# Kernel tuning notes

Measured on AMD Instinct MI355X. Metric: run time of the kernel, lower is better.

## Reference

```python
import jax, jax.numpy as jnp
import numpy as np

DIM = 128
H = 8
HD = DIM // H
NL = 6
DFF = 2048
EPS = 1e-5
S2S_STEPS = 6


def _ln(x, g, b):
    m = jnp.mean(x, -1, keepdims=True)
    v = jnp.mean(jnp.square(x - m), -1, keepdims=True)
    return (x - m) / jnp.sqrt(v + EPS) * g + b


def _lstm_step(x, h, c, wih, whh, bih, bhh):
    # torch LSTM gate order: i, f, g, o
    gates = x @ wih.T + bih + h @ whh.T + bhh
    i, f, g, o = jnp.split(gates, 4, axis=-1)
    c = jax.nn.sigmoid(f) * c + jax.nn.sigmoid(i) * jnp.tanh(g)
    h = jax.nn.sigmoid(o) * jnp.tanh(c)
    return h, c


def setup_inputs() -> dict:
    key = jax.random.key(0)
    ks = iter(jax.random.split(key, 16))
    n = lambda shape: jax.random.normal(next(ks), shape, jnp.float32) * 0.02
    inp = {
        "data": jax.random.normal(next(ks), (64, 256, 3), jnp.float32),
        "lin0_w": n((DIM, 3)), "lin0_b": jnp.zeros((DIM,), jnp.float32),
        "attn_in_w": n((NL, 3 * DIM, DIM)), "attn_in_b": jnp.zeros((NL, 3 * DIM), jnp.float32),
        "attn_out_w": n((NL, DIM, DIM)), "attn_out_b": jnp.zeros((NL, DIM), jnp.float32),
        "ln1_g": jnp.ones((NL, DIM), jnp.float32), "ln1_b": jnp.zeros((NL, DIM), jnp.float32),
        "ff_w1": n((NL, DFF, DIM)), "ff_b1": jnp.zeros((NL, DFF), jnp.float32),
        "ff_w2": n((NL, DIM, DFF)), "ff_b2": jnp.zeros((NL, DIM), jnp.float32),
        "ln2_g": jnp.ones((NL, DIM), jnp.float32), "ln2_b": jnp.zeros((NL, DIM), jnp.float32),
        "s2s_wih": n((4 * DIM, 2 * DIM)), "s2s_whh": n((4 * DIM, DIM)),
        "s2s_bih": jnp.zeros((4 * DIM,), jnp.float32), "s2s_bhh": jnp.zeros((4 * DIM,), jnp.float32),
        "mem_wih": n((4 * DIM, 2 * DIM)), "mem_whh": n((4 * DIM, DIM)),
        "mem_bih": jnp.zeros((4 * DIM,), jnp.float32), "mem_bhh": jnp.zeros((4 * DIM,), jnp.float32),
        "lin1_w": n((DIM, DIM)), "lin1_b": jnp.zeros((DIM,), jnp.float32),
        "lin3_w": n((1, DIM)), "lin3_b": jnp.zeros((1,), jnp.float32),
    }
    return inp


def reference(data, lin0_w, lin0_b, attn_in_w, attn_in_b, attn_out_w, attn_out_b,
              ln1_g, ln1_b, ff_w1, ff_b1, ff_w2, ff_b2, ln2_g, ln2_b,
              s2s_wih, s2s_whh, s2s_bih, s2s_bhh,
              mem_wih, mem_whh, mem_bih, mem_bhh,
              lin1_w, lin1_b, lin3_w, lin3_b):
    x = jax.nn.relu(data @ lin0_w.T + lin0_b)  # [S=64, B=256, D]
    S, B, _ = x.shape
    # torch TransformerEncoder with batch_first=False: attention over axis 0,
    # axis 1 is the transformer batch. Post-norm layers (norm_first=False), relu FFN.
    for l in range(NL):
        qkv = x @ attn_in_w[l].T + attn_in_b[l]
        q, k, v = jnp.split(qkv, 3, axis=-1)
        q = q.reshape(S, B, H, HD)
        k = k.reshape(S, B, H, HD)
        v = v.reshape(S, B, H, HD)
        scores = jnp.einsum('sbhd,tbhd->bhst', q, k) / np.float32(np.sqrt(HD))
        attn = jax.nn.softmax(scores, axis=-1)
        ao = jnp.einsum('bhst,tbhd->sbhd', attn, v).reshape(S, B, DIM)
        x = _ln(x + ao @ attn_out_w[l].T + attn_out_b[l], ln1_g[l], ln1_b[l])
        ff = jax.nn.relu(x @ ff_w1[l].T + ff_b1[l]) @ ff_w2[l].T + ff_b2[l]
        x = _ln(x + ff, ln2_g[l], ln2_b[l])
    # Set2Set pooling: bidxs assign segment = axis-0 index for each block of
    # num_atoms consecutive rows of flatten(out,0,1), i.e. pool over axis 1.
    q_star = jnp.zeros((S, 2 * DIM), x.dtype)
    h = jnp.zeros((S, DIM), x.dtype)
    c = jnp.zeros((S, DIM), x.dtype)
    for _ in range(S2S_STEPS):
        h, c = _lstm_step(q_star, h, c, s2s_wih, s2s_whh, s2s_bih, s2s_bhh)
        e = jnp.einsum('bnd,bd->bn', x, h)          # [S, num_atoms]
        a = jax.nn.softmax(e, axis=-1)              # segment softmax (uniform segs)
        r = jnp.einsum('bn,bnd->bd', a, x)          # segment weighted sum
        q_star = jnp.concatenate([h, r], axis=-1)   # [S, 2D]
    # memory LSTM: seq_len 1, zero initial state (states=None branch)
    hx = jnp.zeros((S, DIM), x.dtype)
    cx = jnp.zeros((S, DIM), x.dtype)
    hx, cx = _lstm_step(q_star, hx, cx, mem_wih, mem_whh, mem_bih, mem_bhh)
    o = jax.nn.relu(hx @ lin1_w.T + lin1_b)
    v_out = (o @ lin3_w.T + lin3_b)[None]  # [1, S, 1]
    return v_out, hx[None], cx[None]
```

## Files before the change

kernel.cpp:

```cpp
#include <hip/hip_runtime.h>
#include <math.h>


typedef __attribute__((ext_vector_type(8))) short bf16x8;
typedef __attribute__((ext_vector_type(4))) float f32x4;
typedef _Float16 __attribute__((ext_vector_type(2))) h16x2;

__device__ __forceinline__ unsigned short f2bf(float f) {
  union { float f; unsigned u; } x; x.f = f;
  unsigned r = x.u + 0x7fff + ((x.u >> 16) & 1);
  return (unsigned short)(r >> 16);
}
__device__ __forceinline__ float uplo(unsigned u) {
  union { unsigned u; float f; } x; x.u = u << 16; return x.f;
}
__device__ __forceinline__ float uphi(unsigned u) {
  union { unsigned u; float f; } x; x.u = u & 0xffff0000u; return x.f;
}
__device__ __forceinline__ unsigned short f2h(float f) {
  union { _Float16 h; unsigned short s; } x; x.h = (_Float16)f; return x.s;
}
__device__ __forceinline__ unsigned packh(float a, float b) {
  return (unsigned)f2h(a) | ((unsigned)f2h(b) << 16);
}
__device__ __forceinline__ float hlo(unsigned u) {
  union { unsigned short s; _Float16 h; } x; x.s = (unsigned short)(u & 0xffff);
  return (float)x.h;
}
__device__ __forceinline__ float hhi(unsigned u) {
  union { unsigned short s; _Float16 h; } x; x.s = (unsigned short)(u >> 16);
  return (float)x.h;
}
__device__ __forceinline__ float fdot2u(unsigned a, unsigned b, float c) {
#if __has_builtin(__builtin_amdgcn_fdot2)
  union U { unsigned u; h16x2 h; };
  U x, y; x.u = a; y.u = b;
  return __builtin_amdgcn_fdot2(x.h, y.h, c, false);
#else
  return c + hlo(a) * hlo(b) + hhi(a) * hhi(b);
#endif
}
__device__ __forceinline__ float sigf(float x) { return 1.f / (1.f + expf(-x)); }

__device__ __forceinline__ void gl2lds16(const void* g, void* l) {
  __builtin_amdgcn_global_load_lds(
      (const __attribute__((address_space(1))) unsigned int*)g,
      (__attribute__((address_space(3))) unsigned int*)l, 16, 0, 0);
}

__global__ __launch_bounds__(256) void convw_kernel(
    const float* __restrict__ aiw, const float* __restrict__ aow,
    const float* __restrict__ w1, const float* __restrict__ w2,
    const float* __restrict__ wih, const float* __restrict__ whh,
    const float* __restrict__ mwih,
    unsigned short* __restrict__ o0, unsigned short* __restrict__ o1,
    unsigned short* __restrict__ o2, unsigned short* __restrict__ o3,
    unsigned short* __restrict__ o4, unsigned short* __restrict__ o5,
    unsigned short* __restrict__ o6) {
  int i = blockIdx.x * 256 + threadIdx.x;
  if (i < 294912) {
    o0[i] = f2bf(aiw[i]);
  } else if (i < 393216) {
    int j = i - 294912; o1[j] = f2bf(aow[j]);
  } else if (i < 1966080) {
    int j = i - 393216; o2[j] = f2bf(w1[j]);
  } else if (i < 3538944) {
    int j = i - 1966080; o3[j] = f2bf(w2[j]);
  } else if (i < 3670016) {
    int j = i - 3538944; o4[j] = f2h(wih[j]);
  } else if (i < 3735552) {
    int j = i - 3670016; o5[j] = f2h(whh[j]);
  } else {
    int j = i - 3735552; o6[j] = f2h(mwih[j]);
  }
}

__global__ __launch_bounds__(256) void lin0_kernel(
    const float* __restrict__ data, const float* __restrict__ w,
    const float* __restrict__ b, float* __restrict__ x,
    unsigned short* __restrict__ xb) {
  int i = blockIdx.x * 256 + threadIdx.x;
  int n = i >> 7, d = i & 127;
  float v = b[d] + data[n * 3 + 0] * w[d * 3 + 0]
                 + data[n * 3 + 1] * w[d * 3 + 1]
                 + data[n * 3 + 2] * w[d * 3 + 2];
  v = fmaxf(v, 0.0f);
  x[i] = v;
  xb[i] = f2bf(v);
}

__global__ __launch_bounds__(512) void layer_kernel(
    const unsigned short* __restrict__ xbg,
    const unsigned short* __restrict__ wqkv, const float* __restrict__ bqkv,
    const unsigned short* __restrict__ wout, const float* __restrict__ bout,
    const float* __restrict__ ln1g, const float* __restrict__ ln1b,
    const unsigned short* __restrict__ w1, const float* __restrict__ b1,
    const unsigned short* __restrict__ w2, const float* __restrict__ b2,
    const float* __restrict__ ln2g, const float* __restrict__ ln2b,
    float* __restrict__ xio, unsigned short* __restrict__ xbo) {
  __shared__ __align__(16) unsigned short Xs[64 * 128];
  __shared__ __align__(16) unsigned short Ws[256 * 128];
  __shared__ __align__(16) unsigned short U1[128 * 128];
  __shared__ __align__(16) unsigned short U2[128 * 128];
  __shared__ __align__(16) uint4 zchunk;
  __shared__ float psum[8][64], psq[8][64];
  __shared__ float2 stats[64];

  unsigned short* Qs = U1;
  unsigned short* Ks2 = U1 + 8192;
  unsigned short* VT = U2;
  unsigned short* AOs = U2 + 8192;
  unsigned short* Hs = U2;

  int tid = threadIdx.x, w = tid >> 6, lane = tid & 63;
  int b = blockIdx.x;
  int r4 = lane >> 4, cs = lane & 15;
  int fr = lane & 15, fq = lane >> 4;

  if (tid == 0) zchunk = make_uint4(0u, 0u, 0u, 0u);

#pragma unroll
  for (int i = 0; i < 2; i++) {
    int issue = w * 2 + i;
    int row = issue * 4 + r4;
    int g = cs ^ (row & 7);
    gl2lds16(xbg + (size_t)(row * 256 + b) * 128 + g * 8,
             (char*)Xs + issue * 1024);
  }
#pragma unroll
  for (int i = 0; i < 8; i++) {
    int issue = w * 8 + i;
    int row = issue * 4 + r4;
    int g = cs ^ (row & 7);
    gl2lds16(wqkv + (size_t)row * 128 + g * 8, (char*)Ws + issue * 1024);
  }
  __syncthreads();

  {
    f32x4 acc[4][2];
#pragma unroll
    for (int i = 0; i < 4; i++)
#pragma unroll
      for (int j = 0; j < 2; j++) acc[i][j] = (f32x4){0.f, 0.f, 0.f, 0.f};
#pragma unroll
    for (int ks = 0; ks < 4; ks++) {
      bf16x8 af[4], bf[2];
#pragma unroll
      for (int mi = 0; mi < 4; mi++) {
        int row = mi * 16 + fr;
        int kq = (ks * 4 + fq) ^ (row & 7);
        af[mi] = *(const bf16x8*)(Xs + row * 128 + kq * 8);
      }
#pragma unroll
      for (int ni = 0; ni < 2; ni++) {
        int wr = (w * 2 + ni) * 16 + fr;
        int kq = (ks * 4 + fq) ^ (wr & 7);
        bf[ni] = *(const bf16x8*)(Ws + wr * 128 + kq * 8);
      }
#pragma unroll
      for (int mi = 0; mi < 4; mi++)
#pragma unroll
        for (int ni = 0; ni < 2; ni++)
          acc[mi][ni] = __builtin_amdgcn_mfma_f32_16x16x32_bf16(
              af[mi], bf[ni], acc[mi][ni], 0, 0, 0);
    }
#pragma unroll
    for (int ni = 0; ni < 2; ni++) {
      int c = (w * 2 + ni) * 16 + fr;
      float bv = bqkv[c];
      unsigned short* dst = (c < 128) ? Qs : Ks2;
      int cc = c & 127;
#pragma unroll
      for (int mi = 0; mi < 4; mi++)
#pragma unroll
        for (int r = 0; r < 4; r++) {
          int row = mi * 16 + fq * 4 + r;
          dst[row * 128 + (((cc >> 3) ^ (row & 7)) << 3) + (cc & 7)] =
              f2bf(acc[mi][ni][r] + bv);
        }
    }
  }
  __syncthreads();

#pragma unroll
  for (int i = 0; i < 4; i++) {
    int issue = w * 4 + i;
    int row = issue * 4 + r4;
    int g = cs ^ (row & 7);
    gl2lds16(wqkv + (size_t)(256 + row) * 128 + g * 8, (char*)Ws + issue * 1024);
  }
  __syncthreads();

  {
    f32x4 acc[4];
#pragma unroll
    for (int i = 0; i < 4; i++) acc[i] = (f32x4){0.f, 0.f, 0.f, 0.f};
#pragma unroll
    for (int ks = 0; ks < 4; ks++) {
      bf16x8 af[4], bf;
#pragma unroll
      for (int mi = 0; mi < 4; mi++) {
        int row = mi * 16 + fr;
        int kq = (ks * 4 + fq) ^ (row & 7);
        af[mi] = *(const bf16x8*)(Xs + row * 128 + kq * 8);
      }
      {
        int wr = w * 16 + fr;
        int kq = (ks * 4 + fq) ^ (wr & 7);
        bf = *(const bf16x8*)(Ws + wr * 128 + kq * 8);
      }
#pragma unroll
      for (int mi = 0; mi < 4; mi++)
        acc[mi] = __builtin_amdgcn_mfma_f32_16x16x32_bf16(af[mi], bf, acc[mi],
                                                          0, 0, 0);
    }
    int f = w * 16 + fr;
    float bv = bqkv[256 + f];
#pragma unroll
    for (int mi = 0; mi < 4; mi++)
#pragma unroll
      for (int r = 0; r < 4; r++) {
        int srow = mi * 16 + fq * 4 + r;
        VT[f * 64 + (((srow >> 3) ^ (f & 7)) << 3) + (srow & 7)] =
            f2bf(acc[mi][r] + bv);
      }
  }
  __syncthreads();

  {
    int h = w;
    unsigned short* Pb = Ws + w * 4096;
    f32x4 sc[4][4];
#pragma unroll
    for (int i = 0; i < 4; i++)
#pragma unroll
      for (int j = 0; j < 4; j++) sc[i][j] = (f32x4){0.f, 0.f, 0.f, 0.f};
    {
      bf16x8 af[4], bf[4];
#pragma unroll
      for (int mi = 0; mi < 4; mi++) {
        int row = mi * 16 + fr;
        const unsigned short* pa =
            (fq < 2) ? (Qs + row * 128 + (((h * 2 + fq) ^ (row & 7)) << 3))
                     : (const unsigned short*)&zchunk;
        af[mi] = *(const bf16x8*)pa;
      }
#pragma unroll
      for (int ti = 0; ti < 4; ti++) {
        int trow = ti * 16 + fr;
        const unsigned short* pb =
            (fq < 2) ? (Ks2 + trow * 128 + (((h * 2 + fq) ^ (trow & 7)) << 3))
                     : (const unsigned short*)&zchunk;
        bf[ti] = *(const bf16x8*)pb;
      }
#pragma unroll
      for (int mi = 0; mi < 4; mi++)
#pragma unroll
        for (int ti = 0; ti < 4; ti++)
          sc[mi][ti] = __builtin_amdgcn_mfma_f32_16x16x32_bf16(
              af[mi], bf[ti], sc[mi][ti], 0, 0, 0);
    }
#pragma unroll
    for (int mi = 0; mi < 4; mi++) {
#pragma unroll
      for (int r = 0; r < 4; r++) {
        float m = -1e30f;
#pragma unroll
        for (int ti = 0; ti < 4; ti++) m = fmaxf(m, sc[mi][ti][r]);
        m = fmaxf(m, __shfl_xor(m, 1, 64));
        m = fmaxf(m, __shfl_xor(m, 2, 64));
        m = fmaxf(m, __shfl_xor(m, 4, 64));
        m = fmaxf(m, __shfl_xor(m, 8, 64));
        m *= 0.25f;
        float ss = 0.f;
#pragma unroll
        for (int ti = 0; ti < 4; ti++) {
          float p = expf(sc[mi][ti][r] * 0.25f - m);
          sc[mi][ti][r] = p;
          ss += p;
        }
        ss += __shfl_xor(ss, 1, 64);
        ss += __shfl_xor(ss, 2, 64);
        ss += __shfl_xor(ss, 4, 64);
        ss += __shfl_xor(ss, 8, 64);
        float inv = 1.f / ss;
        int prow = mi * 16 + fq * 4 + r;
#pragma unroll
        for (int ti = 0; ti < 4; ti++) {
          int t = ti * 16 + fr;
          Pb[prow * 64 + (((t >> 3) ^ (prow & 7)) << 3) + (t & 7)] =
              f2bf(sc[mi][ti][r] * inv);
        }
      }
    }
    f32x4 po[4];
#pragma unroll
    for (int i = 0; i < 4; i++) po[i] = (f32x4){0.f, 0.f, 0.f, 0.f};
#pragma unroll
    for (int ks2 = 0; ks2 < 2; ks2++) {
      bf16x8 af[4], bf;
#pragma unroll
      for (int si = 0; si < 4; si++) {
        int prow = si * 16 + fr;
        int kq = (ks2 * 4 + fq) ^ (prow & 7);
        af[si] = *(const bf16x8*)(Pb + prow * 64 + kq * 8);
      }
      {
        int vrow = h * 16 + fr;
        int kq = (ks2 * 4 + fq) ^ (vrow & 7);
        bf = *(const bf16x8*)(VT + vrow * 64 + kq * 8);
      }
#pragma unroll
      for (int si = 0; si < 4; si++)
        po[si] = __builtin_amdgcn_mfma_f32_16x16x32_bf16(af[si], bf, po[si],
                                                         0, 0, 0);
    }
#pragma unroll
    for (int si = 0; si < 4; si++)
#pragma unroll
      for (int r = 0; r < 4; r++) {
        int arow = si * 16 + fq * 4 + r;
        int c = h * 16 + fr;
        AOs[arow * 128 + (((c >> 3) ^ (arow & 7)) << 3) + (c & 7)] =
            f2bf(po[si][r]);
      }
  }
  __syncthreads();

#pragma unroll
  for (int i = 0; i < 4; i++) {
    int issue = w * 4 + i;
    int row = issue * 4 + r4;
    int g = cs ^ (row & 7);
    gl2lds16(wout + (size_t)row * 128 + g * 8, (char*)Ws + issue * 1024);
  }
  __syncthreads();

  float vvl[4][4];
  {
    f32x4 acc[4];
#pragma unroll
    for (int i = 0; i < 4; i++) acc[i] = (f32x4){0.f, 0.f, 0.f, 0.f};
#pragma unroll
    for (int ks = 0; ks < 4; ks++) {
      bf16x8 af[4], bf;
#pragma unroll
      for (int si = 0; si < 4; si++) {
        int row = si * 16 + fr;
        int kq = (ks * 4 + fq) ^ (row & 7);
        af[si] = *(const bf16x8*)(AOs + row * 128 + kq * 8);
      }
      {
        int wr = w * 16 + fr;
        int kq = (ks * 4 + fq) ^ (wr & 7);
        bf = *(const bf16x8*)(Ws + wr * 128 + kq * 8);
      }
#pragma unroll
      for (int si = 0; si < 4; si++)
        acc[si] = __builtin_amdgcn_mfma_f32_16x16x32_bf16(af[si], bf, acc[si],
                                                          0, 0, 0);
    }
    int c = w * 16 + fr;
    float bv = bout[c];
    float sums[4][4], sqs[4][4];
#pragma unroll
    for (int si = 0; si < 4; si++)
#pragma unroll
      for (int r = 0; r < 4; r++) {
        int row = si * 16 + fq * 4 + r;
        float v = acc[si][r] + bv + xio[(size_t)(row * 256 + b) * 128 + c];
        vvl[si][r] = v;
        sums[si][r] = v;
        sqs[si][r] = v * v;
      }
#pragma unroll
    for (int d = 1; d < 16; d <<= 1) {
#pragma unroll
      for (int si = 0; si < 4; si++)
#pragma unroll
        for (int r = 0; r < 4; r++) {
          sums[si][r] += __shfl_xor(sums[si][r], d, 64);
          sqs[si][r] += __shfl_xor(sqs[si][r], d, 64);
        }
    }
    if (fr == 0) {
#pragma unroll
      for (int si = 0; si < 4; si++)
#pragma unroll
        for (int r = 0; r < 4; r++) {
          int row = si * 16 + fq * 4 + r;
          psum[w][row] = sums[si][r];
          psq[w][row] = sqs[si][r];
        }
    }
    __syncthreads();
    if (tid < 64) {
      float S = 0.f, Q = 0.f;
#pragma unroll
      for (int ww = 0; ww < 8; ww++) { S += psum[ww][tid]; Q += psq[ww][tid]; }
      float m = S * (1.f / 128.f);
      float var = Q * (1.f / 128.f) - m * m;
      stats[tid] = make_float2(m, rsqrtf(var + 1e-5f));
    }
    __syncthreads();
    float gl = ln1g[c], bl = ln1b[c];
#pragma unroll
    for (int si = 0; si < 4; si++)
#pragma unroll
      for (int r = 0; r < 4; r++) {
        int row = si * 16 + fq * 4 + r;
        float2 st = stats[row];
        float y = (vvl[si][r] - st.x) * st.y * gl + bl;
        vvl[si][r] = y;
        Xs[row * 128 + (((c >> 3) ^ (row & 7)) << 3) + (c & 7)] = f2bf(y);
      }
  }

#pragma unroll
  for (int i = 0; i < 4; i++) {
    int issue = w * 4 + i;
    int row = issue * 4 + r4;
    int g = cs ^ (row & 7);
    gl2lds16(w1 + (size_t)row * 128 + g * 8, (char*)Ws + issue * 1024);
    gl2lds16(w2 + (size_t)row * 2048 + g * 8, (char*)U1 + issue * 1024);
  }
  __syncthreads();

  f32x4 acc2[4];
#pragma unroll
  for (int i = 0; i < 4; i++) acc2[i] = (f32x4){0.f, 0.f, 0.f, 0.f};

  for (int c = 0; c < 16; c++) {
    const unsigned short* W1cur = Ws + (c & 1) * 16384;
    f32x4 acc1[4];
#pragma unroll
    for (int i = 0; i < 4; i++) acc1[i] = (f32x4){0.f, 0.f, 0.f, 0.f};
#pragma unroll
    for (int ks = 0; ks < 4; ks++) {
      bf16x8 af[4], bf;
#pragma unroll
      for (int mi = 0; mi < 4; mi++) {
        int row = mi * 16 + fr;
        int kq = (ks * 4 + fq) ^ (row & 7);
        af[mi] = *(const bf16x8*)(Xs + row * 128 + kq * 8);
      }
      {
        int row = w * 16 + fr;
        int kq = (ks * 4 + fq) ^ (row & 7);
        bf = *(const bf16x8*)(W1cur + row * 128 + kq * 8);
      }
#pragma unroll
      for (int mi = 0; mi < 4; mi++)
        acc1[mi] = __builtin_amdgcn_mfma_f32_16x16x32_bf16(af[mi], bf, acc1[mi],
                                                           0, 0, 0);
    }
    if (c < 15) {
#pragma unroll
      for (int i = 0; i < 4; i++) {
        int issue = w * 4 + i;
        int row = issue * 4 + r4;
        int g = cs ^ (row & 7);
        gl2lds16(w1 + (size_t)((c + 1) * 128 + row) * 128 + g * 8,
                 (char*)Ws + ((c + 1) & 1) * 32768 + issue * 1024);
      }
    }
    {
      int col = w * 16 + fr;
      float bv = b1[c * 128 + col];
#pragma unroll
      for (int mi = 0; mi < 4; mi++)
#pragma unroll
        for (int r = 0; r < 4; r++) {
          int row = mi * 16 + fq * 4 + r;
          Hs[row * 136 + col] = f2bf(fmaxf(acc1[mi][r] + bv, 0.f));
        }
    }
    __syncthreads();

#pragma unroll
    for (int ks = 0; ks < 4; ks++) {
      bf16x8 af[4], bf;
#pragma unroll
      for (int si = 0; si < 4; si++) {
        int row = si * 16 + fr;
        af[si] = *(const bf16x8*)(Hs + row * 136 + ks * 32 + fq * 8);
      }
      {
        int row = w * 16 + fr;
        int kq = (ks * 4 + fq) ^ (row & 7);
        bf = *(const bf16x8*)(U1 + row * 128 + kq * 8);
      }
#pragma unroll
      for (int si = 0; si < 4; si++)
        acc2[si] = __builtin_amdgcn_mfma_f32_16x16x32_bf16(af[si], bf, acc2[si],
                                                           0, 0, 0);
    }
    __syncthreads();
    if (c < 15) {
#pragma unroll
      for (int i = 0; i < 4; i++) {
        int issue = w * 4 + i;
        int row = issue * 4 + r4;
        int g = cs ^ (row & 7);
        gl2lds16(w2 + (size_t)row * 2048 + (c + 1) * 128 + g * 8,
                 (char*)U1 + issue * 1024);
      }
    }
  }

  {
    int c = w * 16 + fr;
    float bv = b2[c];
    float sums[4][4], sqs[4][4];
#pragma unroll
    for (int si = 0; si < 4; si++)
#pragma unroll
      for (int r = 0; r < 4; r++) {
        float v = acc2[si][r] + bv + vvl[si][r];
        vvl[si][r] = v;
        sums[si][r] = v;
        sqs[si][r] = v * v;
      }
#pragma unroll
    for (int d = 1; d < 16; d <<= 1) {
#pragma unroll
      for (int si = 0; si < 4; si++)
#pragma unroll
        for (int r = 0; r < 4; r++) {
          sums[si][r] += __shfl_xor(sums[si][r], d, 64);
          sqs[si][r] += __shfl_xor(sqs[si][r], d, 64);
        }
    }
    if (fr == 0) {
#pragma unroll
      for (int si = 0; si < 4; si++)
#pragma unroll
        for (int r = 0; r < 4; r++) {
          int row = si * 16 + fq * 4 + r;
          psum[w][row] = sums[si][r];
          psq[w][row] = sqs[si][r];
        }
    }
    __syncthreads();
    if (tid < 64) {
      float S = 0.f, Q = 0.f;
#pragma unroll
      for (int ww = 0; ww < 8; ww++) { S += psum[ww][tid]; Q += psq[ww][tid]; }
      float m = S * (1.f / 128.f);
      float var = Q * (1.f / 128.f) - m * m;
      stats[tid] = make_float2(m, rsqrtf(var + 1e-5f));
    }
    __syncthreads();
    float gl = ln2g[c], bl = ln2b[c];
#pragma unroll
    for (int si = 0; si < 4; si++)
#pragma unroll
      for (int r = 0; r < 4; r++) {
        int row = si * 16 + fq * 4 + r;
        float2 st = stats[row];
        float y = (vvl[si][r] - st.x) * st.y * gl + bl;
        size_t o = (size_t)(row * 256 + b) * 128 + c;
        xio[o] = y;
        xbo[o] = f2bf(y);
      }
  }
}

__global__ __launch_bounds__(512, 1) void s2s_kernel(
    const unsigned short* __restrict__ xb,
    const unsigned short* __restrict__ wihh,
    const unsigned short* __restrict__ whhh,
    const float* __restrict__ bih, const float* __restrict__ bhh,
    const unsigned short* __restrict__ mwihh,
    const float* __restrict__ mbih, const float* __restrict__ mbhh,
    const float* __restrict__ l1w, const float* __restrict__ l1b,
    const float* __restrict__ l3w, const float* __restrict__ l3b,
    float* __restrict__ out) {
  __shared__ __align__(16) unsigned xl[256 * 65];
  __shared__ __align__(16) unsigned qu[128];
  __shared__ __align__(16) float cst[128];
  __shared__ __align__(16) float gates[512];
  __shared__ __align__(16) float red[256];
  __shared__ __align__(16) float aw[256];
  int s = blockIdx.x, t = threadIdx.x, lane = t & 63, w = t >> 6;

  uint4 wreg[32], ureg[16];
  {
    const uint4* wp = (const uint4*)(wihh + (size_t)t * 256);
#pragma unroll
    for (int i = 0; i < 32; i++) wreg[i] = wp[i];
    const uint4* up = (const uint4*)(whhh + (size_t)t * 128);
#pragma unroll
    for (int i = 0; i < 16; i++) ureg[i] = up[i];
  }

  const uint4* xs4 = (const uint4*)(xb + (size_t)s * 32768);
#pragma unroll
  for (int it = 0; it < 8; it++) {
    int f = it * 512 + t;
    uint4 v = xs4[f];
    int n = f >> 4, jc = (f & 15) * 4;
    unsigned* dst = xl + n * 65 + jc;
    dst[0] = packh(uplo(v.x), uphi(v.x));
    dst[1] = packh(uplo(v.y), uphi(v.y));
    dst[2] = packh(uplo(v.z), uphi(v.z));
    dst[3] = packh(uplo(v.w), uphi(v.w));
  }
  if (t < 128) cst[t] = 0.f;
  __syncthreads();

  const uint4* q4 = (const uint4*)qu;
  float bsum = bih[t] + bhh[t];

  for (int step = 0; step < 6; step++) {
    if (step > 0) {
      float a0 = 0.f, a1 = 0.f, a2 = 0.f, a3 = 0.f;
#pragma unroll
      for (int i = 0; i < 16; i++) {
        uint4 qv = q4[i];
        a0 = fdot2u(wreg[i].x, qv.x, a0);
        a1 = fdot2u(wreg[i].y, qv.y, a1);
        a2 = fdot2u(wreg[i].z, qv.z, a2);
        a3 = fdot2u(wreg[i].w, qv.w, a3);
        a0 = fdot2u(ureg[i].x, qv.x, a0);
        a1 = fdot2u(ureg[i].y, qv.y, a1);
        a2 = fdot2u(ureg[i].z, qv.z, a2);
        a3 = fdot2u(ureg[i].w, qv.w, a3);
      }
#pragma unroll
      for (int i = 16; i < 32; i++) {
        uint4 qv = q4[i];
        a0 = fdot2u(wreg[i].x, qv.x, a0);
        a1 = fdot2u(wreg[i].y, qv.y, a1);
        a2 = fdot2u(wreg[i].z, qv.z, a2);
        a3 = fdot2u(wreg[i].w, qv.w, a3);
      }
      gates[t] = bsum + ((a0 + a1) + (a2 + a3));
    } else {
      gates[t] = bsum;
    }
    __syncthreads();
    if (t < 128) {
      float ig = sigf(gates[t]), fg = sigf(gates[128 + t]);
      float gg = tanhf(gates[256 + t]), og = sigf(gates[384 + t]);
      float cn = fg * cst[t] + ig * gg;
      cst[t] = cn;
      float hn = og * tanhf(cn);
      float hp = __shfl_xor(hn, 1, 64);
      if ((t & 1) == 0) qu[t >> 1] = packh(hn, hp);
    }
    __syncthreads();
    if (step > 0) {
      int n = t >> 1, p = t & 1;
      const unsigned* xr = xl + n * 65 + p * 32;
      float e0 = 0.f, e1 = 0.f;
#pragma unroll 8
      for (int i = 0; i < 32; i += 2) {
        e0 = fdot2u(xr[i], qu[p * 32 + i], e0);
        e1 = fdot2u(xr[i + 1], qu[p * 32 + i + 1], e1);
      }
      float e = e0 + e1;
      e += __shfl_xor(e, 1, 64);
      if (p == 0) red[n] = e;
      __syncthreads();
      float v0 = red[lane], v1 = red[64 + lane];
      float v2 = red[128 + lane], v3 = red[192 + lane];
      float m = fmaxf(fmaxf(v0, v1), fmaxf(v2, v3));
#pragma unroll
      for (int d = 1; d < 64; d <<= 1) m = fmaxf(m, __shfl_xor(m, d, 64));
      float p0 = expf(v0 - m), p1 = expf(v1 - m);
      float p2 = expf(v2 - m), p3 = expf(v3 - m);
      float ss = p0 + p1 + p2 + p3;
#pragma unroll
      for (int d = 1; d < 64; d <<= 1) ss += __shfl_xor(ss, d, 64);
      float Sinv = 1.f / ss;
      if (w == 0) {
        aw[lane] = p0 * Sinv; aw[64 + lane] = p1 * Sinv;
        aw[128 + lane] = p2 * Sinv; aw[192 + lane] = p3 * Sinv;
      }
    } else {
      if (t < 256) aw[t] = 1.f / 256.f;
    }
    __syncthreads();
    {
      int d = t & 127, grp = t >> 7;
      const unsigned* xc = xl + grp * 64 * 65 + (d >> 1);
      int hi = d & 1;
      const float* ap = aw + grp * 64;
      float r = 0.f;
#pragma unroll 8
      for (int n2 = 0; n2 < 64; n2++) {
        unsigned u = xc[n2 * 65];
        r += ap[n2] * (hi ? hhi(u) : hlo(u));
      }
      gates[t] = r;
    }
    __syncthreads();
    if (t < 128) {
      float rd = gates[t] + gates[128 + t] + gates[256 + t] + gates[384 + t];
      float rp = __shfl_xor(rd, 1, 64);
      if ((t & 1) == 0) qu[64 + (t >> 1)] = packh(rd, rp);
    }
    __syncthreads();
  }
  {
    float a0 = 0.f, a1 = 0.f, a2 = 0.f, a3 = 0.f;
    const uint4* mp = (const uint4*)(mwihh + (size_t)t * 256);
#pragma unroll 8
    for (int i = 0; i < 32; i++) {
      uint4 wv = mp[i], qv = q4[i];
      a0 = fdot2u(wv.x, qv.x, a0);
      a1 = fdot2u(wv.y, qv.y, a1);
      a2 = fdot2u(wv.z, qv.z, a2);
      a3 = fdot2u(wv.w, qv.w, a3);
    }
    gates[t] = mbih[t] + mbhh[t] + ((a0 + a1) + (a2 + a3));
  }
  __syncthreads();
  if (t < 128) {
    float ig = sigf(gates[t]);
    float gg = tanhf(gates[256 + t]);
    float og = sigf(gates[384 + t]);
    float cx = ig * gg;
    float hx = og * tanhf(cx);
    cst[t] = hx;
    out[64 + s * 128 + t] = hx;
    out[64 + 8192 + s * 128 + t] = cx;
  }
  __syncthreads();
  if (t < 128) {
    float acc = l1b[t];
    const float4* w4 = (const float4*)(l1w + (size_t)t * 128);
    const float4* h4 = (const float4*)cst;
#pragma unroll 8
    for (int k = 0; k < 32; k++) {
      float4 a = w4[k], b = h4[k];
      acc += a.x * b.x + a.y * b.y + a.z * b.z + a.w * b.w;
    }
    red[t] = fmaxf(acc, 0.f) * l3w[t];
  } else if (t < 256) {
    red[t] = 0.f;
  }
  __syncthreads();
  for (int off = 128; off; off >>= 1) {
    if (t < off) red[t] += red[t + off];
    __syncthreads();
  }
  if (t == 0) out[s] = red[0] + l3b[0];
}

extern "C" void kernel_launch(void* const* d_in, const int* in_sizes, int n_in,
                              void* d_out, int out_size, void* d_ws,
                              size_t ws_size, hipStream_t stream) {
  const float* data       = (const float*)d_in[0];
  const float* lin0_w     = (const float*)d_in[1];
  const float* lin0_b     = (const float*)d_in[2];
  const float* attn_in_w  = (const float*)d_in[3];
  const float* attn_in_b  = (const float*)d_in[4];
  const float* attn_out_w = (const float*)d_in[5];
  const float* attn_out_b = (const float*)d_in[6];
  const float* ln1_g      = (const float*)d_in[7];
  const float* ln1_b      = (const float*)d_in[8];
  const float* ff_w1      = (const float*)d_in[9];
  const float* ff_b1      = (const float*)d_in[10];
  const float* ff_w2      = (const float*)d_in[11];
  const float* ff_b2      = (const float*)d_in[12];
  const float* ln2_g      = (const float*)d_in[13];
  const float* ln2_b      = (const float*)d_in[14];
  const float* s2s_wih    = (const float*)d_in[15];
  const float* s2s_whh    = (const float*)d_in[16];
  const float* s2s_bih    = (const float*)d_in[17];
  const float* s2s_bhh    = (const float*)d_in[18];
  const float* mem_wih    = (const float*)d_in[19];
  const float* mem_bih    = (const float*)d_in[21];
  const float* mem_bhh    = (const float*)d_in[22];
  const float* lin1_w     = (const float*)d_in[23];
  const float* lin1_b     = (const float*)d_in[24];
  const float* lin3_w     = (const float*)d_in[25];
  const float* lin3_b     = (const float*)d_in[26];
  float* out = (float*)d_out;

  char* p = (char*)d_ws;
  float* x = (float*)p;                      p += (size_t)16384 * 128 * 4;
  unsigned short* xb = (unsigned short*)p;   p += (size_t)16384 * 128 * 2;
  unsigned short* wqkv = (unsigned short*)p; p += (size_t)294912 * 2;
  unsigned short* wout = (unsigned short*)p; p += (size_t)98304 * 2;
  unsigned short* w1b = (unsigned short*)p;  p += (size_t)1572864 * 2;
  unsigned short* w2b = (unsigned short*)p;  p += (size_t)1572864 * 2;
  unsigned short* wihh = (unsigned short*)p; p += (size_t)131072 * 2;
  unsigned short* whhh = (unsigned short*)p; p += (size_t)65536 * 2;
  unsigned short* mwihh = (unsigned short*)p; p += (size_t)131072 * 2;

  convw_kernel<<<15104, 256, 0, stream>>>(
      attn_in_w, attn_out_w, ff_w1, ff_w2, s2s_wih, s2s_whh, mem_wih,
      wqkv, wout, w1b, w2b, wihh, whhh, mwihh);
  lin0_kernel<<<8192, 256, 0, stream>>>(data, lin0_w, lin0_b, x, xb);

  for (int l = 0; l < 6; l++) {
    layer_kernel<<<256, 512, 0, stream>>>(
        xb, wqkv + (size_t)l * 49152, attn_in_b + l * 384,
        wout + (size_t)l * 16384, attn_out_b + l * 128,
        ln1_g + l * 128, ln1_b + l * 128,
        w1b + (size_t)l * 262144, ff_b1 + l * 2048,
        w2b + (size_t)l * 262144, ff_b2 + l * 128,
        ln2_g + l * 128, ln2_b + l * 128, x, xb);
  }

  s2s_kernel<<<64, 512, 0, stream>>>(
      xb, wihh, whhh, s2s_bih, s2s_bhh,
      mwihh, mem_bih, mem_bhh, lin1_w, lin1_b, lin3_w, lin3_b, out);
}
```

Measured before the change: 504.0 us.

## Keep FFN hidden activations in registers via transposed fp16 MFMA chaining

Result: slower. 530.2 us (+5.2%).

```diff
diff --git a/kernel.cpp b/kernel.cpp
--- a/kernel.cpp
+++ b/kernel.cpp
@@ -5,11 +5,16 @@
 typedef __attribute__((ext_vector_type(8))) short bf16x8;
 typedef __attribute__((ext_vector_type(4))) float f32x4;
 typedef _Float16 __attribute__((ext_vector_type(2))) h16x2;
+typedef _Float16 __attribute__((ext_vector_type(4))) f16x4;
 
 __device__ __forceinline__ unsigned short f2bf(float f) {
   union { float f; unsigned u; } x; x.f = f;
   unsigned r = x.u + 0x7fff + ((x.u >> 16) & 1);
   return (unsigned short)(r >> 16);
+}
+__device__ __forceinline__ float bf2f(unsigned short u) {
+  union { unsigned u; float f; } x; x.u = ((unsigned)u) << 16;
+  return x.f;
 }
 __device__ __forceinline__ float uplo(unsigned u) {
   union { unsigned u; float f; } x; x.u = u << 16; return x.f;
@@ -65,7 +70,7 @@
   } else if (i < 1966080) {
     int j = i - 393216; o2[j] = f2bf(w1[j]);
   } else if (i < 3538944) {
-    int j = i - 1966080; o3[j] = f2bf(w2[j]);
+    int j = i - 1966080; o3[j] = f2h(w2[j]);
   } else if (i < 3670016) {
     int j = i - 3538944; o4[j] = f2h(wih[j]);
   } else if (i < 3735552) {
@@ -110,7 +115,6 @@
   unsigned short* Ks2 = U1 + 8192;
   unsigned short* VT = U2;
   unsigned short* AOs = U2 + 8192;
-  unsigned short* Hs = U2;
 
   int tid = threadIdx.x, w = tid >> 6, lane = tid & 63;
   int b = blockIdx.x;
@@ -336,7 +340,6 @@
   }
   __syncthreads();
 
-  float vvl[4][4];
   {
     f32x4 acc[4];
 #pragma unroll
@@ -362,6 +365,7 @@
     }
     int c = w * 16 + fr;
     float bv = bout[c];
+    float vv4[4][4];
     float sums[4][4], sqs[4][4];
 #pragma unroll
     for (int si = 0; si < 4; si++)
@@ -369,7 +373,7 @@
       for (int r = 0; r < 4; r++) {
         int row = si * 16 + fq * 4 + r;
         float v = acc[si][r] + bv + xio[(size_t)(row * 256 + b) * 128 + c];
-        vvl[si][r] = v;
+        vv4[si][r] = v;
         sums[si][r] = v;
         sqs[si][r] = v * v;
       }
@@ -394,6 +398,15 @@
         }
     }
     __syncthreads();
+
+#pragma unroll
+    for (int i = 0; i < 4; i++) {
+      int issue = w * 4 + i;
+      int row = issue * 4 + r4;
+      int g = cs ^ (row & 7);
+      gl2lds16(w1 + (size_t)row * 128 + g * 8, (char*)Ws + issue * 1024);
+      gl2lds16(w2 + (size_t)row * 2048 + g * 8, (char*)U1 + issue * 1024);
+    }
     if (tid < 64) {
       float S = 0.f, Q = 0.f;
 #pragma unroll
@@ -409,51 +422,23 @@
 #pragma unroll
       for (int r = 0; r < 4; r++) {
         int row = si * 16 + fq * 4 + r;
-        float2 st = stats[row];
-        float y = (vvl[si][r] - st.x) * st.y * gl + bl;
-        vvl[si][r] = y;
+        float2 st2 = stats[row];
+        float y = (vv4[si][r] - st2.x) * st2.y * gl + bl;
         Xs[row * 128 + (((c >> 3) ^ (row & 7)) << 3) + (c & 7)] = f2bf(y);
       }
   }
-
-#pragma unroll
-  for (int i = 0; i < 4; i++) {
-    int issue = w * 4 + i;
-    int row = issue * 4 + r4;
-    int g = cs ^ (row & 7);
-    gl2lds16(w1 + (size_t)row * 128 + g * 8, (char*)Ws + issue * 1024);
-    gl2lds16(w2 + (size_t)row * 2048 + g * 8, (char*)U1 + issue * 1024);
-  }
-  __syncthreads();
-
-  f32x4 acc2[4];
-#pragma unroll
-  for (int i = 0; i < 4; i++) acc2[i] = (f32x4){0.f, 0.f, 0.f, 0.f};
+  __syncthreads();
+
+  int st = w >> 1;
+  int hh = w & 1;
+
+  f32x4 acc2[8];
+#pragma unroll
+  for (int i = 0; i < 8; i++) acc2[i] = (f32x4){0.f, 0.f, 0.f, 0.f};
 
   for (int c = 0; c < 16; c++) {
     const unsigned short* W1cur = Ws + (c & 1) * 16384;
-    f32x4 acc1[4];
-#pragma unroll
-    for (int i = 0; i < 4; i++) acc1[i] = (f32x4){0.f, 0.f, 0.f, 0.f};
-#pragma unroll
-    for (int ks = 0; ks < 4; ks++) {
-      bf16x8 af[4], bf;
-#pragma unroll
-      for (int mi = 0; mi < 4; mi++) {
-        int row = mi * 16 + fr;
-        int kq = (ks * 4 + fq) ^ (row & 7);
-        af[mi] = *(const bf16x8*)(Xs + row * 128 + kq * 8);
-      }
-      {
-        int row = w * 16 + fr;
-        int kq = (ks * 4 + fq) ^ (row & 7);
-        bf = *(const bf16x8*)(W1cur + row * 128 + kq * 8);
-      }
-#pragma unroll
-      for (int mi = 0; mi < 4; mi++)
-        acc1[mi] = __builtin_amdgcn_mfma_f32_16x16x32_bf16(af[mi], bf, acc1[mi],
-                                                           0, 0, 0);
-    }
+    const unsigned short* W2cur = (c & 1) ? U2 : U1;
     if (c < 15) {
 #pragma unroll
       for (int i = 0; i < 4; i++) {
@@ -462,107 +447,94 @@
         int g = cs ^ (row & 7);
         gl2lds16(w1 + (size_t)((c + 1) * 128 + row) * 128 + g * 8,
                  (char*)Ws + ((c + 1) & 1) * 32768 + issue * 1024);
-      }
-    }
-    {
-      int col = w * 16 + fr;
-      float bv = b1[c * 128 + col];
-#pragma unroll
-      for (int mi = 0; mi < 4; mi++)
-#pragma unroll
-        for (int r = 0; r < 4; r++) {
-          int row = mi * 16 + fq * 4 + r;
-          Hs[row * 136 + col] = f2bf(fmaxf(acc1[mi][r] + bv, 0.f));
-        }
-    }
-    __syncthreads();
-
-#pragma unroll
-    for (int ks = 0; ks < 4; ks++) {
-      bf16x8 af[4], bf;
-#pragma unroll
-      for (int si = 0; si < 4; si++) {
-        int row = si * 16 + fr;
-        af[si] = *(const bf16x8*)(Hs + row * 136 + ks * 32 + fq * 8);
-      }
-      {
-        int row = w * 16 + fr;
-        int kq = (ks * 4 + fq) ^ (row & 7);
-        bf = *(const bf16x8*)(U1 + row * 128 + kq * 8);
-      }
-#pragma unroll
-      for (int si = 0; si < 4; si++)
-        acc2[si] = __builtin_amdgcn_mfma_f32_16x16x32_bf16(af[si], bf, acc2[si],
-                                                           0, 0, 0);
-    }
-    __syncthreads();
-    if (c < 15) {
-#pragma unroll
-      for (int i = 0; i < 4; i++) {
-        int issue = w * 4 + i;
-        int row = issue * 4 + r4;
-        int g = cs ^ (row & 7);
         gl2lds16(w2 + (size_t)row * 2048 + (c + 1) * 128 + g * 8,
-                 (char*)U1 + issue * 1024);
-      }
-    }
-  }
-
-  {
-    int c = w * 16 + fr;
-    float bv = b2[c];
-    float sums[4][4], sqs[4][4];
-#pragma unroll
-    for (int si = 0; si < 4; si++)
-#pragma unroll
-      for (int r = 0; r < 4; r++) {
-        float v = acc2[si][r] + bv + vvl[si][r];
-        vvl[si][r] = v;
-        sums[si][r] = v;
-        sqs[si][r] = v * v;
-      }
-#pragma unroll
-    for (int d = 1; d < 16; d <<= 1) {
-#pragma unroll
-      for (int si = 0; si < 4; si++)
-#pragma unroll
-        for (int r = 0; r < 4; r++) {
-          sums[si][r] += __shfl_xor(sums[si][r], d, 64);
-          sqs[si][r] += __shfl_xor(sqs[si][r], d, 64);
-        }
-    }
-    if (fr == 0) {
-#pragma unroll
-      for (int si = 0; si < 4; si++)
-#pragma unroll
-        for (int r = 0; r < 4; r++) {
-          int row = si * 16 + fq * 4 + r;
-          psum[w][row] = sums[si][r];
-          psq[w][row] = sqs[si][r];
-        }
-    }
-    __syncthreads();
-    if (tid < 64) {
-      float S = 0.f, Q = 0.f;
-#pragma unroll
-      for (int ww = 0; ww < 8; ww++) { S += psum[ww][tid]; Q += psq[ww][tid]; }
-      float m = S * (1.f / 128.f);
-      float var = Q * (1.f / 128.f) - m * m;
-      stats[tid] = make_float2(m, rsqrtf(var + 1e-5f));
-    }
-    __syncthreads();
-    float gl = ln2g[c], bl = ln2b[c];
-#pragma unroll
-    for (int si = 0; si < 4; si++)
-#pragma unroll
-      for (int r = 0; r < 4; r++) {
-        int row = si * 16 + fq * 4 + r;
-        float2 st = stats[row];
-        float y = (vvl[si][r] - st.x) * st.y * gl + bl;
-        size_t o = (size_t)(row * 256 + b) * 128 + c;
-        xio[o] = y;
-        xbo[o] = f2bf(y);
-      }
+                 (char*)((c & 1) ? U1 : U2) + issue * 1024);
+      }
+    }
+    f16x4 hf[4];
+#pragma unroll
+    for (int ht = 0; ht < 4; ht++) {
+      f32x4 a1 = (f32x4){0.f, 0.f, 0.f, 0.f};
+      int hrow = hh * 64 + ht * 16 + fr;
+      int srow = st * 16 + fr;
+#pragma unroll
+      for (int ks = 0; ks < 4; ks++) {
+        bf16x8 aw = *(const bf16x8*)(W1cur + hrow * 128 +
+                                     (((ks * 4 + fq) ^ (hrow & 7)) << 3));
+        bf16x8 bx = *(const bf16x8*)(Xs + srow * 128 +
+                                     (((ks * 4 + fq) ^ (srow & 7)) << 3));
+        a1 = __builtin_amdgcn_mfma_f32_16x16x32_bf16(aw, bx, a1, 0, 0, 0);
+      }
+      float4 b1v = *(const float4*)(b1 + c * 128 + hh * 64 + ht * 16 + fq * 4);
+      hf[ht][0] = (_Float16)fmaxf(a1[0] + b1v.x, 0.f);
+      hf[ht][1] = (_Float16)fmaxf(a1[1] + b1v.y, 0.f);
+      hf[ht][2] = (_Float16)fmaxf(a1[2] + b1v.z, 0.f);
+      hf[ht][3] = (_Float16)fmaxf(a1[3] + b1v.w, 0.f);
+    }
+#pragma unroll
+    for (int ot = 0; ot < 8; ot++) {
+#pragma unroll
+      for (int ht = 0; ht < 4; ht++) {
+        int orow = ot * 16 + fr;
+        int c16 = hh * 8 + ht * 2 + (fq >> 1);
+        f16x4 wv = *(const f16x4*)(W2cur + orow * 128 +
+                                   ((c16 ^ (orow & 7)) << 3) + (fq & 1) * 4);
+        acc2[ot] = __builtin_amdgcn_mfma_f32_16x16x16f16(wv, hf[ht], acc2[ot],
+                                                         0, 0, 0);
+      }
+    }
+    __syncthreads();
+  }
+
+  if (hh == 1) {
+    float* slot = (float*)Ws + st * 2048;
+#pragma unroll
+    for (int ot = 0; ot < 8; ot++)
+      *(f32x4*)(slot + ot * 256 + lane * 4) = acc2[ot];
+  }
+  __syncthreads();
+  if (hh == 0) {
+    const float* slot = (const float*)Ws + st * 2048;
+#pragma unroll
+    for (int ot = 0; ot < 8; ot++)
+      acc2[ot] += *(const f32x4*)(slot + ot * 256 + lane * 4);
+
+    int s = st * 16 + fr;
+    float vals[8][4];
+    float sum = 0.f, sq = 0.f;
+#pragma unroll
+    for (int ot = 0; ot < 8; ot++) {
+      int o0 = ot * 16 + fq * 4;
+      float4 b2v = *(const float4*)(b2 + o0);
+      int cx = ((o0 >> 3) ^ (s & 7));
+      ushort4 ru = *(const ushort4*)(Xs + s * 128 + (cx << 3) + (fq & 1) * 4);
+      float v0 = acc2[ot][0] + b2v.x + bf2f(ru.x);
+      float v1 = acc2[ot][1] + b2v.y + bf2f(ru.y);
+      float v2 = acc2[ot][2] + b2v.z + bf2f(ru.z);
+      float v3 = acc2[ot][3] + b2v.w + bf2f(ru.w);
+      vals[ot][0] = v0; vals[ot][1] = v1; vals[ot][2] = v2; vals[ot][3] = v3;
+      sum += (v0 + v1) + (v2 + v3);
+      sq += (v0 * v0 + v1 * v1) + (v2 * v2 + v3 * v3);
+    }
+    sum += __shfl_xor(sum, 16, 64); sum += __shfl_xor(sum, 32, 64);
+    sq += __shfl_xor(sq, 16, 64);   sq += __shfl_xor(sq, 32, 64);
+    float mean = sum * (1.f / 128.f);
+    float inv = rsqrtf(sq * (1.f / 128.f) - mean * mean + 1e-5f);
+    size_t rowbase = (size_t)(s * 256 + b) * 128;
+#pragma unroll
+    for (int ot = 0; ot < 8; ot++) {
+      int o0 = ot * 16 + fq * 4;
+      float4 g4 = *(const float4*)(ln2g + o0);
+      float4 bb4 = *(const float4*)(ln2b + o0);
+      float y0 = (vals[ot][0] - mean) * inv * g4.x + bb4.x;
+      float y1 = (vals[ot][1] - mean) * inv * g4.y + bb4.y;
+      float y2 = (vals[ot][2] - mean) * inv * g4.z + bb4.z;
+      float y3 = (vals[ot][3] - mean) * inv * g4.w + bb4.w;
+      *(float4*)(xio + rowbase + o0) = make_float4(y0, y1, y2, y3);
+      ushort4 ub;
+      ub.x = f2bf(y0); ub.y = f2bf(y1); ub.z = f2bf(y2); ub.w = f2bf(y3);
+      *(ushort4*)(xbo + rowbase + o0) = ub;
+    }
   }
 }
 
@@ -786,14 +758,14 @@
   unsigned short* wqkv = (unsigned short*)p; p += (size_t)294912 * 2;
   unsigned short* wout = (unsigned short*)p; p += (size_t)98304 * 2;
   unsigned short* w1b = (unsigned short*)p;  p += (size_t)1572864 * 2;
-  unsigned short* w2b = (unsigned short*)p;  p += (size_t)1572864 * 2;
+  unsigned short* w2h = (unsigned short*)p;  p += (size_t)1572864 * 2;
   unsigned short* wihh = (unsigned short*)p; p += (size_t)131072 * 2;
   unsigned short* whhh = (unsigned short*)p; p += (size_t)65536 * 2;
   unsigned short* mwihh = (unsigned short*)p; p += (size_t)131072 * 2;
 
   convw_kernel<<<15104, 256, 0, stream>>>(
       attn_in_w, attn_out_w, ff_w1, ff_w2, s2s_wih, s2s_whh, mem_wih,
-      wqkv, wout, w1b, w2b, wihh, whhh, mwihh);
+      wqkv, wout, w1b, w2h, wihh, whhh, mwihh);
   lin0_kernel<<<8192, 256, 0, stream>>>(data, lin0_w, lin0_b, x, xb);
 
   for (int l = 0; l < 6; l++) {
@@ -802,7 +774,7 @@
         wout + (size_t)l * 16384, attn_out_b + l * 128,
         ln1_g + l * 128, ln1_b + l * 128,
         w1b + (size_t)l * 262144, ff_b1 + l * 2048,
-        w2b + (size_t)l * 262144, ff_b2 + l * 128,
+        w2h + (size_t)l * 262144, ff_b2 + l * 128,
         ln2_g + l * 128, ln2_b + l * 128, x, xb);
   }
 
```

## Cache X fragments in registers, swizzle FFN hidden tile, prefetch FFN weights earlier

Applied to the files above, without the earlier changes.

Result: faster. 487.9 us (-3.2%).

```diff
diff --git a/kernel.cpp b/kernel.cpp
--- a/kernel.cpp
+++ b/kernel.cpp
@@ -136,6 +136,16 @@
   }
   __syncthreads();
 
+  bf16x8 xfragA[4][4];
+#pragma unroll
+  for (int ks = 0; ks < 4; ks++)
+#pragma unroll
+    for (int mi = 0; mi < 4; mi++) {
+      int row = mi * 16 + fr;
+      int kq = (ks * 4 + fq) ^ (row & 7);
+      xfragA[ks][mi] = *(const bf16x8*)(Xs + row * 128 + kq * 8);
+    }
+
   {
     f32x4 acc[4][2];
 #pragma unroll
@@ -144,13 +154,7 @@
       for (int j = 0; j < 2; j++) acc[i][j] = (f32x4){0.f, 0.f, 0.f, 0.f};
 #pragma unroll
     for (int ks = 0; ks < 4; ks++) {
-      bf16x8 af[4], bf[2];
-#pragma unroll
-      for (int mi = 0; mi < 4; mi++) {
-        int row = mi * 16 + fr;
-        int kq = (ks * 4 + fq) ^ (row & 7);
-        af[mi] = *(const bf16x8*)(Xs + row * 128 + kq * 8);
-      }
+      bf16x8 bf[2];
 #pragma unroll
       for (int ni = 0; ni < 2; ni++) {
         int wr = (w * 2 + ni) * 16 + fr;
@@ -162,7 +166,7 @@
 #pragma unroll
         for (int ni = 0; ni < 2; ni++)
           acc[mi][ni] = __builtin_amdgcn_mfma_f32_16x16x32_bf16(
-              af[mi], bf[ni], acc[mi][ni], 0, 0, 0);
+              xfragA[ks][mi], bf[ni], acc[mi][ni], 0, 0, 0);
     }
 #pragma unroll
     for (int ni = 0; ni < 2; ni++) {
@@ -197,13 +201,7 @@
     for (int i = 0; i < 4; i++) acc[i] = (f32x4){0.f, 0.f, 0.f, 0.f};
 #pragma unroll
     for (int ks = 0; ks < 4; ks++) {
-      bf16x8 af[4], bf;
-#pragma unroll
-      for (int mi = 0; mi < 4; mi++) {
-        int row = mi * 16 + fr;
-        int kq = (ks * 4 + fq) ^ (row & 7);
-        af[mi] = *(const bf16x8*)(Xs + row * 128 + kq * 8);
-      }
+      bf16x8 bf;
       {
         int wr = w * 16 + fr;
         int kq = (ks * 4 + fq) ^ (wr & 7);
@@ -211,8 +209,8 @@
       }
 #pragma unroll
       for (int mi = 0; mi < 4; mi++)
-        acc[mi] = __builtin_amdgcn_mfma_f32_16x16x32_bf16(af[mi], bf, acc[mi],
-                                                          0, 0, 0);
+        acc[mi] = __builtin_amdgcn_mfma_f32_16x16x32_bf16(xfragA[ks][mi], bf,
+                                                          acc[mi], 0, 0, 0);
     }
     int f = w * 16 + fr;
     float bv = bqkv[256 + f];
@@ -336,7 +334,6 @@
   }
   __syncthreads();
 
-  float vvl[4][4];
   {
     f32x4 acc[4];
 #pragma unroll
@@ -362,6 +359,7 @@
     }
     int c = w * 16 + fr;
     float bv = bout[c];
+    float vv4[4][4];
     float sums[4][4], sqs[4][4];
 #pragma unroll
     for (int si = 0; si < 4; si++)
@@ -369,7 +367,7 @@
       for (int r = 0; r < 4; r++) {
         int row = si * 16 + fq * 4 + r;
         float v = acc[si][r] + bv + xio[(size_t)(row * 256 + b) * 128 + c];
-        vvl[si][r] = v;
+        vv4[si][r] = v;
         sums[si][r] = v;
         sqs[si][r] = v * v;
       }
@@ -394,6 +392,15 @@
         }
     }
     __syncthreads();
+
+#pragma unroll
+    for (int i = 0; i < 4; i++) {
+      int issue = w * 4 + i;
+      int row = issue * 4 + r4;
+      int g = cs ^ (row & 7);
+      gl2lds16(w1 + (size_t)row * 128 + g * 8, (char*)Ws + issue * 1024);
+      gl2lds16(w2 + (size_t)row * 2048 + g * 8, (char*)U1 + issue * 1024);
+    }
     if (tid < 64) {
       float S = 0.f, Q = 0.f;
 #pragma unroll
@@ -409,22 +416,22 @@
 #pragma unroll
       for (int r = 0; r < 4; r++) {
         int row = si * 16 + fq * 4 + r;
-        float2 st = stats[row];
-        float y = (vvl[si][r] - st.x) * st.y * gl + bl;
-        vvl[si][r] = y;
+        float2 st2 = stats[row];
+        float y = (vv4[si][r] - st2.x) * st2.y * gl + bl;
         Xs[row * 128 + (((c >> 3) ^ (row & 7)) << 3) + (c & 7)] = f2bf(y);
       }
   }
-
-#pragma unroll
-  for (int i = 0; i < 4; i++) {
-    int issue = w * 4 + i;
-    int row = issue * 4 + r4;
-    int g = cs ^ (row & 7);
-    gl2lds16(w1 + (size_t)row * 128 + g * 8, (char*)Ws + issue * 1024);
-    gl2lds16(w2 + (size_t)row * 2048 + g * 8, (char*)U1 + issue * 1024);
-  }
-  __syncthreads();
+  __syncthreads();
+
+  bf16x8 xfragF[4][4];
+#pragma unroll
+  for (int ks = 0; ks < 4; ks++)
+#pragma unroll
+    for (int mi = 0; mi < 4; mi++) {
+      int row = mi * 16 + fr;
+      int kq = (ks * 4 + fq) ^ (row & 7);
+      xfragF[ks][mi] = *(const bf16x8*)(Xs + row * 128 + kq * 8);
+    }
 
   f32x4 acc2[4];
 #pragma unroll
@@ -437,13 +444,7 @@
     for (int i = 0; i < 4; i++) acc1[i] = (f32x4){0.f, 0.f, 0.f, 0.f};
 #pragma unroll
     for (int ks = 0; ks < 4; ks++) {
-      bf16x8 af[4], bf;
-#pragma unroll
-      for (int mi = 0; mi < 4; mi++) {
-        int row = mi * 16 + fr;
-        int kq = (ks * 4 + fq) ^ (row & 7);
-        af[mi] = *(const bf16x8*)(Xs + row * 128 + kq * 8);
-      }
+      bf16x8 bf;
       {
         int row = w * 16 + fr;
         int kq = (ks * 4 + fq) ^ (row & 7);
@@ -451,8 +452,8 @@
       }
 #pragma unroll
       for (int mi = 0; mi < 4; mi++)
-        acc1[mi] = __builtin_amdgcn_mfma_f32_16x16x32_bf16(af[mi], bf, acc1[mi],
-                                                           0, 0, 0);
+        acc1[mi] = __builtin_amdgcn_mfma_f32_16x16x32_bf16(xfragF[ks][mi], bf,
+                                                           acc1[mi], 0, 0, 0);
     }
     if (c < 15) {
 #pragma unroll
@@ -472,7 +473,8 @@
 #pragma unroll
         for (int r = 0; r < 4; r++) {
           int row = mi * 16 + fq * 4 + r;
-          Hs[row * 136 + col] = f2bf(fmaxf(acc1[mi][r] + bv, 0.f));
+          Hs[row * 128 + (((col >> 3) ^ (row & 7)) << 3) + (col & 7)] =
+              f2bf(fmaxf(acc1[mi][r] + bv, 0.f));
         }
     }
     __syncthreads();
@@ -483,7 +485,8 @@
 #pragma unroll
       for (int si = 0; si < 4; si++) {
         int row = si * 16 + fr;
-        af[si] = *(const bf16x8*)(Hs + row * 136 + ks * 32 + fq * 8);
+        int kq = (ks * 4 + fq) ^ (row & 7);
+        af[si] = *(const bf16x8*)(Hs + row * 128 + kq * 8);
       }
       {
         int row = w * 16 + fr;
@@ -511,13 +514,17 @@
   {
     int c = w * 16 + fr;
     float bv = b2[c];
+    float vv4[4][4];
     float sums[4][4], sqs[4][4];
 #pragma unroll
     for (int si = 0; si < 4; si++)
 #pragma unroll
       for (int r = 0; r < 4; r++) {
-        float v = acc2[si][r] + bv + vvl[si][r];
-        vvl[si][r] = v;
+        int row = si * 16 + fq * 4 + r;
+        float resid = uplo((unsigned)
+            Xs[row * 128 + (((c >> 3) ^ (row & 7)) << 3) + (c & 7)]);
+        float v = acc2[si][r] + bv + resid;
+        vv4[si][r] = v;
         sums[si][r] = v;
         sqs[si][r] = v * v;
       }
@@ -558,7 +565,7 @@
       for (int r = 0; r < 4; r++) {
         int row = si * 16 + fq * 4 + r;
         float2 st = stats[row];
-        float y = (vvl[si][r] - st.x) * st.y * gl + bl;
+        float y = (vv4[si][r] - st.x) * st.y * gl + bl;
         size_t o = (size_t)(row * 256 + b) * 128 + c;
         xio[o] = y;
         xbo[o] = f2bf(y);
```
